# Optimization experiments

Hardware: AMD Instinct MI355X
Metric: run time of the kernel (lower is better)

The kernel has to match this reference:

```python
import jax, jax.numpy as jnp
import numpy as np

D = 192          # d_model
H = 8            # n_heads
DH = D // H      # d_head = 24
DFF = 2 * D      # FeedForward hidden = d_model*2
SIZES = [384 + 8 * i for i in range(32)]   # ragged segment lengths
TOTAL = sum(SIZES)                          # 16256
EPS = 1e-5

# static ragged -> padded index maps (numpy, baked at trace time)
_sz = np.asarray(SIZES)
B = len(_sz)
MAXN = int(_sz.max())
SEG = np.repeat(np.arange(B), _sz)                      # [TOTAL] segment id
POS = np.concatenate([np.arange(s) for s in _sz])       # [TOTAL] position in segment
PADMASK = np.ones((B, MAXN), dtype=bool)                # True = padding (key_padding_mask)
PADMASK[SEG, POS] = False


def _layernorm(x, gamma, beta):
    mu = jnp.mean(x, axis=-1, keepdims=True)
    var = jnp.var(x, axis=-1, keepdims=True)
    return (x - mu) * jax.lax.rsqrt(var + EPS) * gamma + beta


def setup_inputs() -> dict:
    key = jax.random.key(0)
    ks = jax.random.split(key, 8)
    w = lambda k, shape: jax.random.normal(k, shape, jnp.float32) * 0.02
    return {
        "x": jax.random.normal(ks[0], (TOTAL, D), jnp.float32),
        "sizes": jnp.asarray(SIZES, jnp.int32),
        "Wqkv": w(ks[1], (3 * D, D)), "bqkv": jnp.zeros((3 * D,), jnp.float32),
        "Wo": w(ks[2], (D, D)),       "bo": jnp.zeros((D,), jnp.float32),
        "Wg": w(ks[3], (D, 2 * D)),   "bg": jnp.zeros((D,), jnp.float32),
        "gamma1": jnp.ones((D,), jnp.float32), "beta1": jnp.zeros((D,), jnp.float32),
        "W1": w(ks[4], (DFF, D)),     "b1": jnp.zeros((DFF,), jnp.float32),
        "W2": w(ks[5], (D, DFF)),     "b2": jnp.zeros((D,), jnp.float32),
        "gamma2": jnp.ones((D,), jnp.float32), "beta2": jnp.zeros((D,), jnp.float32),
    }


def reference(x, sizes, Wqkv, bqkv, Wo, bo, Wg, bg, gamma1, beta1,
              W1, b1, W2, b2, gamma2, beta2):
    # --- pad_by_sizes (vectorized scatter, static index maps) ---
    pad = jnp.zeros((B, MAXN, D), x.dtype).at[SEG, POS].set(x)   # [B, MAXN, D]

    # --- nn.MultiheadAttention (batch_first, key_padding_mask) ---
    qkv = pad @ Wqkv.T + bqkv                                    # [B, MAXN, 3D]
    q, k, v = jnp.split(qkv, 3, axis=-1)
    def heads(t):  # [B, MAXN, D] -> [B, H, MAXN, DH]
        return t.reshape(B, MAXN, H, DH).transpose(0, 2, 1, 3)
    q, k, v = heads(q), heads(k), heads(v)
    scores = jnp.einsum("bhqd,bhkd->bhqk", q, k) / np.sqrt(DH)   # [B, H, MAXN, MAXN]
    scores = jnp.where(PADMASK[:, None, None, :], jnp.float32(-1e9), scores)
    attn = jax.nn.softmax(scores, axis=-1)
    o = jnp.einsum("bhqk,bhkd->bhqd", attn, v)                   # [B, H, MAXN, DH]
    o = o.transpose(0, 2, 1, 3).reshape(B, MAXN, D)
    out = o @ Wo.T + bo                                          # [B, MAXN, D]

    # --- gather back to ragged; gate/norm/ff are per-token, so the torch
    # per-segment loop is equivalent to one vectorized pass over all tokens ---
    out_flat = out[SEG, POS]                                     # [TOTAL, D]
    g = jax.nn.sigmoid(jnp.concatenate([out_flat, x], axis=-1) @ Wg.T + bg)
    h = g * out_flat + (1.0 - g) * x                             # GatedResidual
    h = _layernorm(h, gamma1, beta1)                             # self.norm
    y = jax.nn.silu(h @ W1.T + b1) @ W2.T + b2                   # FeedForward.net
    return _layernorm(h + y, gamma2, beta2)                      # residual + norm
```

## Files before the change

kernel.cpp:

```cpp
#include <hip/hip_runtime.h>
#include <math.h>

#define D_      192
#define H_      8
#define DH_     24
#define NSEG    32
#define TOTAL_  16256
static constexpr float LN_EPS = 1e-5f;
static constexpr float SCALE  = 0.20412414523193154f;
static constexpr float SC_L2E = 0.29446679331797463f;

typedef float  f32x4  __attribute__((ext_vector_type(4)));
typedef short  bf16x8 __attribute__((ext_vector_type(8)));
typedef unsigned short u16x4 __attribute__((ext_vector_type(4)));

__device__ __forceinline__ unsigned short f2b(float f) {
    union { float f; unsigned u; } v; v.f = f;
    unsigned r = v.u + 0x7FFFu + ((v.u >> 16) & 1u);
    return (unsigned short)(r >> 16);
}
__device__ __forceinline__ unsigned short f2b_fast(float f) {
    union { float f; unsigned u; } v; v.f = f;
    return (unsigned short)((v.u + 0x8000u) >> 16);
}
__device__ __forceinline__ float b2f(unsigned short h) {
    union { unsigned u; float f; } v; v.u = (unsigned)h << 16; return v.f;
}
__device__ __forceinline__ float fexp2(float x) {
#if __has_builtin(__builtin_amdgcn_exp2f)
    return __builtin_amdgcn_exp2f(x);
#else
    return exp2f(x);
#endif
}
__device__ __forceinline__ bf16x8 ldpack8(const float* p) {
    float4 a0 = *(const float4*)p;
    float4 a1 = *(const float4*)(p + 4);
    bf16x8 r;
    ((unsigned short*)&r)[0] = f2b(a0.x); ((unsigned short*)&r)[1] = f2b(a0.y);
    ((unsigned short*)&r)[2] = f2b(a0.z); ((unsigned short*)&r)[3] = f2b(a0.w);
    ((unsigned short*)&r)[4] = f2b(a1.x); ((unsigned short*)&r)[5] = f2b(a1.y);
    ((unsigned short*)&r)[6] = f2b(a1.z); ((unsigned short*)&r)[7] = f2b(a1.w);
    return r;
}

__global__ __launch_bounds__(256)
void conv_w(const float* __restrict__ w0, const float* __restrict__ w1,
            const float* __restrict__ w2, const float* __restrict__ w3,
            const float* __restrict__ w4, unsigned short* __restrict__ out)
{
    int i = (blockIdx.x * 256 + threadIdx.x) * 4;
    const float* src; int off;
    if      (i < 110592) { src = w0; off = 0; }
    else if (i < 147456) { src = w1; off = 110592; }
    else if (i < 221184) { src = w2; off = 147456; }
    else if (i < 294912) { src = w3; off = 221184; }
    else                 { src = w4; off = 294912; }
    float4 v = *(const float4*)&src[i - off];
    u16x4 o = { f2b(v.x), f2b(v.y), f2b(v.z), f2b(v.w) };
    *(u16x4*)&out[i] = o;
}

template<int KF, int MR, int OUT_BF16, int AF32>
__global__ __launch_bounds__(256)
void gemm_lds(const void* __restrict__ Ain,
              const unsigned short* __restrict__ Wb,
              const float* __restrict__ bias,
              void* __restrict__ Cout, int N)
{
    constexpr int KSW = KF * 32 + 8;
    __shared__ unsigned short Wp[64 * KSW];

    const int tid = threadIdx.x;
    const int wv  = tid >> 6;
    const int l   = tid & 63;
    const int m0  = blockIdx.x * (64 * MR) + wv * (16 * MR);
    const int n0  = blockIdx.y * 64;
    const int rl  = l & 15;
    const int kc  = (l >> 4) * 8;

    bf16x8 afrag[MR][KF];
    #pragma unroll
    for (int h = 0; h < MR; ++h)
        #pragma unroll
        for (int kk = 0; kk < KF; ++kk) {
            if (AF32)
                afrag[h][kk] = ldpack8((const float*)Ain + (size_t)(m0 + h * 16 + rl) * (KF * 32) + kk * 32 + kc);
            else
                afrag[h][kk] = *(const bf16x8*)((const unsigned short*)Ain + (size_t)(m0 + h * 16 + rl) * (KF * 32) + kk * 32 + kc);
        }

    #pragma unroll
    for (int i = 0; i < KF; ++i) {
        int u = i * 256 + tid;
        int row = u / (KF * 4), c = u % (KF * 4);
        *(bf16x8*)&Wp[row * KSW + c * 8] = *(const bf16x8*)&Wb[(size_t)(n0 + row) * (KF * 32) + c * 8];
    }
    __syncthreads();

    f32x4 acc[MR][4] = {};
    #pragma unroll
    for (int kk = 0; kk < KF; ++kk) {
        #pragma unroll
        for (int nf = 0; nf < 4; ++nf) {
            bf16x8 b = *(const bf16x8*)&Wp[(nf * 16 + rl) * KSW + kk * 32 + kc];
            #pragma unroll
            for (int h = 0; h < MR; ++h)
                acc[h][nf] = __builtin_amdgcn_mfma_f32_16x16x32_bf16(afrag[h][kk], b, acc[h][nf], 0, 0, 0);
        }
    }

    #pragma unroll
    for (int h = 0; h < MR; ++h) {
        #pragma unroll
        for (int nf = 0; nf < 4; ++nf) {
            const int c = n0 + nf * 16 + rl;
            const float bz = bias[c];
            #pragma unroll
            for (int q = 0; q < 4; ++q) {
                const int r = m0 + h * 16 + (l >> 4) * 4 + q;
                float v = acc[h][nf][q] + bz;
                if (OUT_BF16) ((unsigned short*)Cout)[(size_t)r * N + c] = f2b(v);
                else          ((float*)Cout)[(size_t)r * N + c] = v;
            }
        }
    }
}

__global__ __launch_bounds__(256, 1)
void wo_gate_ln1(const unsigned short* __restrict__ o_b,
                 const float* __restrict__ x,
                 const unsigned short* __restrict__ wo_b,
                 const unsigned short* __restrict__ wg_b,
                 const float* __restrict__ bo, const float* __restrict__ bg,
                 const float* __restrict__ gamma1, const float* __restrict__ beta1,
                 float* __restrict__ h1, unsigned short* __restrict__ h1b)
{
    constexpr int WS = 200;
    constexpr int AS = 200;
    __shared__ unsigned short Wp[192 * WS];
    __shared__ unsigned short Al[64 * AS];

    const int tid = threadIdx.x;
    const int wv  = tid >> 6;
    const int l   = tid & 63;
    const int rl  = l & 15;
    const int g   = l >> 4;
    const int kc  = g * 8;
    const int blk0 = blockIdx.x * 64;
    const int m0   = blk0 + wv * 16;

    bf16x8 afA[6];
    #pragma unroll
    for (int kk = 0; kk < 6; ++kk)
        afA[kk] = *(const bf16x8*)&o_b[(size_t)(m0 + rl) * 192 + kk * 32 + kc];

    #pragma unroll
    for (int i = 0; i < 18; ++i) {
        int u = i * 256 + tid;
        int row = u / 24, c = u % 24;
        *(bf16x8*)&Wp[row * WS + c * 8] = *(const bf16x8*)&wo_b[(size_t)row * 192 + c * 8];
    }
    __syncthreads();

    f32x4 accA[12] = {};
    #pragma unroll
    for (int kk = 0; kk < 6; ++kk)
        #pragma unroll
        for (int nf = 0; nf < 12; ++nf) {
            bf16x8 b = *(const bf16x8*)&Wp[(nf * 16 + rl) * WS + kk * 32 + kc];
            accA[nf] = __builtin_amdgcn_mfma_f32_16x16x32_bf16(afA[kk], b, accA[nf], 0, 0, 0);
        }

    float att[12][4];
    #pragma unroll
    for (int nf = 0; nf < 12; ++nf) {
        const float bz = bo[nf * 16 + rl];
        #pragma unroll
        for (int q = 0; q < 4; ++q) {
            att[nf][q] = accA[nf][q] + bz;
            const int row = wv * 16 + g * 4 + q;
            Al[row * AS + nf * 16 + rl] = f2b(att[nf][q]);
        }
    }
    __syncthreads();

    #pragma unroll
    for (int i = 0; i < 18; ++i) {
        int u = i * 256 + tid;
        int row = u / 24, c = u % 24;
        *(bf16x8*)&Wp[row * WS + c * 8] = *(const bf16x8*)&wg_b[(size_t)row * 384 + c * 8];
    }
    __syncthreads();

    f32x4 accB[12] = {};
    #pragma unroll
    for (int kk = 0; kk < 6; ++kk) {
        bf16x8 a = *(const bf16x8*)&Al[(wv * 16 + rl) * AS + kk * 32 + kc];
        #pragma unroll
        for (int nf = 0; nf < 12; ++nf) {
            bf16x8 b = *(const bf16x8*)&Wp[(nf * 16 + rl) * WS + kk * 32 + kc];
            accB[nf] = __builtin_amdgcn_mfma_f32_16x16x32_bf16(a, b, accB[nf], 0, 0, 0);
        }
    }
    __syncthreads();

    #pragma unroll
    for (int i = 0; i < 18; ++i) {
        int u = i * 256 + tid;
        int row = u / 24, c = u % 24;
        *(bf16x8*)&Wp[row * WS + c * 8] = *(const bf16x8*)&wg_b[(size_t)row * 384 + 192 + c * 8];
    }
    __syncthreads();

    #pragma unroll
    for (int kk = 0; kk < 6; ++kk) {
        bf16x8 a = ldpack8(&x[(size_t)(m0 + rl) * 192 + kk * 32 + kc]);
        #pragma unroll
        for (int nf = 0; nf < 12; ++nf) {
            bf16x8 b = *(const bf16x8*)&Wp[(nf * 16 + rl) * WS + kk * 32 + kc];
            accB[nf] = __builtin_amdgcn_mfma_f32_16x16x32_bf16(a, b, accB[nf], 0, 0, 0);
        }
    }

    float bz[12], gam[12], bet[12];
    #pragma unroll
    for (int nf = 0; nf < 12; ++nf) {
        bz[nf]  = bg[nf * 16 + rl];
        gam[nf] = gamma1[nf * 16 + rl];
        bet[nf] = beta1[nf * 16 + rl];
    }
    #pragma unroll
    for (int q = 0; q < 4; ++q) {
        const int r = m0 + g * 4 + q;
        const size_t rb = (size_t)r * 192;
        float h[12];
        float s = 0.f;
        #pragma unroll
        for (int nf = 0; nf < 12; ++nf) {
            const int c = nf * 16 + rl;
            float v  = accB[nf][q] + bz[nf];
            float gt = 1.f / (1.f + __expf(-v));
            h[nf] = gt * att[nf][q] + (1.f - gt) * x[rb + c];
            s += h[nf];
        }
        s += __shfl_xor(s, 1); s += __shfl_xor(s, 2);
        s += __shfl_xor(s, 4); s += __shfl_xor(s, 8);
        const float mu = s * (1.f / 192.f);
        float sq = 0.f;
        #pragma unroll
        for (int nf = 0; nf < 12; ++nf) { float d = h[nf] - mu; sq += d * d; }
        sq += __shfl_xor(sq, 1); sq += __shfl_xor(sq, 2);
        sq += __shfl_xor(sq, 4); sq += __shfl_xor(sq, 8);
        const float rstd = rsqrtf(sq * (1.f / 192.f) + LN_EPS);
        #pragma unroll
        for (int nf = 0; nf < 12; ++nf) {
            const int c = nf * 16 + rl;
            float rv = (h[nf] - mu) * rstd * gam[nf] + bet[nf];
            h1[rb + c]  = rv;
            h1b[rb + c] = f2b(rv);
        }
    }
}

__global__ __launch_bounds__(256, 1)
void ffn_ln2(const unsigned short* __restrict__ h1b,
             const float* __restrict__ h1,
             const unsigned short* __restrict__ w1_b,
             const unsigned short* __restrict__ w2_b,
             const float* __restrict__ b1, const float* __restrict__ b2,
             const float* __restrict__ gamma2, const float* __restrict__ beta2,
             float* __restrict__ out)
{
    constexpr int WS = 200;
    constexpr int FS = 392;
    __shared__ unsigned short Wp[192 * WS];
    __shared__ unsigned short Fl[64 * FS];

    const int tid = threadIdx.x;
    const int wv  = tid >> 6;
    const int l   = tid & 63;
    const int rl  = l & 15;
    const int g   = l >> 4;
    const int kc  = g * 8;
    const int blk0 = blockIdx.x * 64;
    const int m0   = blk0 + wv * 16;

    bf16x8 afC[6];
    #pragma unroll
    for (int kk = 0; kk < 6; ++kk)
        afC[kk] = *(const bf16x8*)&h1b[(size_t)(m0 + rl) * 192 + kk * 32 + kc];

    f32x4 accC[24] = {};
    #pragma unroll
    for (int ch = 0; ch < 2; ++ch) {
        if (ch) __syncthreads();
        #pragma unroll
        for (int i = 0; i < 18; ++i) {
            int u = i * 256 + tid;
            int row = u / 24, c = u % 24;
            *(bf16x8*)&Wp[row * WS + c * 8] = *(const bf16x8*)&w1_b[(size_t)(ch * 192 + row) * 192 + c * 8];
        }
        __syncthreads();
        #pragma unroll
        for (int kk = 0; kk < 6; ++kk)
            #pragma unroll
            for (int nf = 0; nf < 12; ++nf) {
                bf16x8 b = *(const bf16x8*)&Wp[(nf * 16 + rl) * WS + kk * 32 + kc];
                accC[ch * 12 + nf] = __builtin_amdgcn_mfma_f32_16x16x32_bf16(afC[kk], b, accC[ch * 12 + nf], 0, 0, 0);
            }
    }
    #pragma unroll
    for (int ch = 0; ch < 2; ++ch)
        #pragma unroll
        for (int nf = 0; nf < 12; ++nf) {
            const int col = ch * 192 + nf * 16 + rl;
            const float bz = b1[col];
            #pragma unroll
            for (int q = 0; q < 4; ++q) {
                float v = accC[ch * 12 + nf][q] + bz;
                float s = 1.f / (1.f + __expf(-v));
                const int row = wv * 16 + g * 4 + q;
                Fl[row * FS + col] = f2b(v * s);
            }
        }
    __syncthreads();

    f32x4 accD[12] = {};
    #pragma unroll
    for (int ch = 0; ch < 2; ++ch) {
        if (ch) __syncthreads();
        #pragma unroll
        for (int i = 0; i < 18; ++i) {
            int u = i * 256 + tid;
            int row = u / 24, c = u % 24;
            *(bf16x8*)&Wp[row * WS + c * 8] = *(const bf16x8*)&w2_b[(size_t)row * 384 + ch * 192 + c * 8];
        }
        __syncthreads();
        #pragma unroll
        for (int kk = 0; kk < 6; ++kk) {
            bf16x8 a = *(const bf16x8*)&Fl[(wv * 16 + rl) * FS + ch * 192 + kk * 32 + kc];
            #pragma unroll
            for (int nf = 0; nf < 12; ++nf) {
                bf16x8 b = *(const bf16x8*)&Wp[(nf * 16 + rl) * WS + kk * 32 + kc];
                accD[nf] = __builtin_amdgcn_mfma_f32_16x16x32_bf16(a, b, accD[nf], 0, 0, 0);
            }
        }
    }

    float bz[12], gam[12], bet[12];
    #pragma unroll
    for (int nf = 0; nf < 12; ++nf) {
        bz[nf]  = b2[nf * 16 + rl];
        gam[nf] = gamma2[nf * 16 + rl];
        bet[nf] = beta2[nf * 16 + rl];
    }
    #pragma unroll
    for (int q = 0; q < 4; ++q) {
        const int r = m0 + g * 4 + q;
        const size_t rb = (size_t)r * 192;
        float h[12];
        float s = 0.f;
        #pragma unroll
        for (int nf = 0; nf < 12; ++nf) {
            const int c = nf * 16 + rl;
            h[nf] = h1[rb + c] + accD[nf][q] + bz[nf];
            s += h[nf];
        }
        s += __shfl_xor(s, 1); s += __shfl_xor(s, 2);
        s += __shfl_xor(s, 4); s += __shfl_xor(s, 8);
        const float mu = s * (1.f / 192.f);
        float sq = 0.f;
        #pragma unroll
        for (int nf = 0; nf < 12; ++nf) { float d = h[nf] - mu; sq += d * d; }
        sq += __shfl_xor(sq, 1); sq += __shfl_xor(sq, 2);
        sq += __shfl_xor(sq, 4); sq += __shfl_xor(sq, 8);
        const float rstd = rsqrtf(sq * (1.f / 192.f) + LN_EPS);
        #pragma unroll
        for (int nf = 0; nf < 12; ++nf) {
            const int c = nf * 16 + rl;
            out[rb + c] = (h[nf] - mu) * rstd * gam[nf] + bet[nf];
        }
    }
}

#define KSTR 40
#define VSTR 72
#define PSTR 72

__global__ __launch_bounds__(256)
void attn_mfma(const unsigned short* __restrict__ qkv, unsigned short* __restrict__ o)
{
    const int seg  = blockIdx.z;
    const int head = blockIdx.y;
    const int n    = 384 + 8 * seg;
    const int base = 384 * seg + 4 * seg * (seg - 1);
    const int q0   = blockIdx.x * 128;
    if (q0 >= n) return;

    __shared__ unsigned short Ks[64 * KSTR];
    __shared__ unsigned short Vt[32 * VSTR];
    __shared__ unsigned short Pl[4][32 * PSTR];

    const int tid = threadIdx.x;
    const int wv  = tid >> 6;
    const int l   = tid & 63;
    const int lq  = l & 15;
    const int g   = l >> 4;

    if (tid < 64) *(uint4*)&Ks[tid * KSTR + 24] = make_uint4(0, 0, 0, 0);
    for (int t4 = tid; t4 < 144; t4 += 256)
        *(unsigned long long*)&Vt[24 * VSTR + t4 * 4] = 0ull;

    int   qrow[2];
    bf16x8 qfrag[2];
    #pragma unroll
    for (int qf = 0; qf < 2; ++qf) {
        qrow[qf] = q0 + wv * 32 + qf * 16 + lq;
        const int qtok = base + (qrow[qf] < n ? qrow[qf] : n - 1);
        bf16x8 qz = {};
        if (g < 3) qz = *(const bf16x8*)&qkv[(size_t)qtok * 576 + head * 24 + g * 8];
        qfrag[qf] = qz;
    }

    float lsum[2] = {0.f, 0.f};
    f32x4 oacc[2][2] = {};

    const int nt = (n + 63) >> 6;
    for (int t = 0; t < nt; ++t) {
        const int j0 = t * 64;
        __syncthreads();
        if (tid < 192) {
            const int j = tid & 63;
            const int c = tid >> 6;
            int jr = j0 + j; if (jr >= n) jr = n - 1;
            const unsigned short* rp = &qkv[(size_t)(base + jr) * 576 + head * 24 + c * 8];
            bf16x8 kv = *(const bf16x8*)(rp + 192);
            *(bf16x8*)&Ks[j * KSTR + c * 8] = kv;
            bf16x8 vv = *(const bf16x8*)(rp + 384);
            #pragma unroll
            for (int e = 0; e < 8; ++e)
                Vt[(c * 8 + e) * VSTR + j] = ((const unsigned short*)&vv)[e];
        }
        __syncthreads();

        const int rem = n - j0;
        #pragma unroll
        for (int qf = 0; qf < 2; ++qf) {
            f32x4 sacc[4] = {};
            #pragma unroll
            for (int ks = 0; ks < 4; ++ks) {
                bf16x8 kf = *(const bf16x8*)&Ks[(ks * 16 + lq) * KSTR + g * 8];
                sacc[ks] = __builtin_amdgcn_mfma_f32_16x16x32_bf16(kf, qfrag[qf], sacc[ks], 0, 0, 0);
            }
            float psum = 0.f;
            unsigned short pb[16];
            #pragma unroll
            for (int ks = 0; ks < 4; ++ks) {
                #pragma unroll
                for (int r = 0; r < 4; ++r) {
                    float p = fexp2(sacc[ks][r] * SC_L2E);
                    if (rem < 64) { int key = ks * 16 + g * 4 + r; if (key >= rem) p = 0.f; }
                    psum += p;
                    pb[ks * 4 + r] = f2b_fast(p);
                }
            }
            psum += __shfl_xor(psum, 16);
            psum += __shfl_xor(psum, 32);
            lsum[qf] += psum;
            #pragma unroll
            for (int ks = 0; ks < 4; ++ks) {
                u16x4 w4 = { pb[ks*4+0], pb[ks*4+1], pb[ks*4+2], pb[ks*4+3] };
                *(u16x4*)&Pl[wv][(qf * 16 + lq) * PSTR + ks * 16 + g * 4] = w4;
            }
        }
        asm volatile("s_waitcnt lgkmcnt(0)" ::: "memory");
        __builtin_amdgcn_sched_barrier(0);

        #pragma unroll
        for (int jk = 0; jk < 2; ++jk) {
            bf16x8 vf[2];
            #pragma unroll
            for (int df = 0; df < 2; ++df)
                vf[df] = *(const bf16x8*)&Vt[(df * 16 + lq) * VSTR + jk * 32 + g * 8];
            #pragma unroll
            for (int qf = 0; qf < 2; ++qf) {
                bf16x8 pf = *(const bf16x8*)&Pl[wv][(qf * 16 + lq) * PSTR + jk * 32 + g * 8];
                #pragma unroll
                for (int df = 0; df < 2; ++df)
                    oacc[qf][df] = __builtin_amdgcn_mfma_f32_16x16x32_bf16(vf[df], pf, oacc[qf][df], 0, 0, 0);
            }
        }
    }

    #pragma unroll
    for (int qf = 0; qf < 2; ++qf) {
        if (qrow[qf] < n) {
            const float rl2 = 1.f / lsum[qf];
            #pragma unroll
            for (int df = 0; df < 2; ++df) {
                const int d0 = df * 16 + g * 4;
                if (d0 < 24) {
                    u16x4 r = { f2b_fast(oacc[qf][df][0] * rl2), f2b_fast(oacc[qf][df][1] * rl2),
                                f2b_fast(oacc[qf][df][2] * rl2), f2b_fast(oacc[qf][df][3] * rl2) };
                    *(u16x4*)&o[(size_t)(base + qrow[qf]) * 192 + head * 24 + d0] = r;
                }
            }
        }
    }
}

extern "C" void kernel_launch(void* const* d_in, const int* in_sizes, int n_in,
                              void* d_out, int out_size, void* d_ws, size_t ws_size,
                              hipStream_t stream)
{
    const float* x      = (const float*)d_in[0];
    const float* Wqkv   = (const float*)d_in[2];
    const float* bqkv   = (const float*)d_in[3];
    const float* Wo     = (const float*)d_in[4];
    const float* bo     = (const float*)d_in[5];
    const float* Wg     = (const float*)d_in[6];
    const float* bg     = (const float*)d_in[7];
    const float* gamma1 = (const float*)d_in[8];
    const float* beta1  = (const float*)d_in[9];
    const float* W1     = (const float*)d_in[10];
    const float* b1     = (const float*)d_in[11];
    const float* W2     = (const float*)d_in[12];
    const float* b2     = (const float*)d_in[13];
    const float* gamma2 = (const float*)d_in[14];
    const float* beta2  = (const float*)d_in[15];
    float* out = (float*)d_out;
    float* ws  = (float*)d_ws;

    const size_t T = TOTAL_;
    unsigned short* qkv_b = (unsigned short*)ws;
    unsigned short* o_b   = (unsigned short*)(ws + 288 * T);
    float*          h1    = ws + 384 * T;
    unsigned short* h1b   = (unsigned short*)(ws + 576 * T);
    unsigned short* wb    = (unsigned short*)(ws + 672 * T);

    dim3 blk(256);

    conv_w<<<dim3(360), blk, 0, stream>>>(Wqkv, Wo, Wg, W1, W2, wb);
    gemm_lds<6,2,1,1><<<dim3(127, 9), blk, 0, stream>>>(x, wb, bqkv, qkv_b, 576);
    attn_mfma<<<dim3(5, H_, NSEG), blk, 0, stream>>>(qkv_b, o_b);
    wo_gate_ln1<<<dim3(254), blk, 0, stream>>>(o_b, x, wb + 110592, wb + 147456,
                                               bo, bg, gamma1, beta1, h1, h1b);
    ffn_ln2<<<dim3(254), blk, 0, stream>>>(h1b, h1, wb + 221184, wb + 294912,
                                           b1, b2, gamma2, beta2, out);
}
```

Measured before the change: 105.1 us.

## Keep attention P in registers via permuted V layout; pre-convert x to bf16

In the attention kernel, the softmax probabilities are packed straight into registers as the B operand of the PV MFMA. This removes the per-wave LDS round trip and its waitcnt barrier, and works because V is stored transposed with a column permutation that matches the accumulator layout of the score MFMA. K fragments are also hoisted out of the q-fragment loop. Separately, x is converted to bf16 once in the weight-conversion kernel, so the QKV GEMM loads bf16 directly instead of converting fp32 in every one of its 9 column blocks. That adds an extra pass over x and a larger conversion launch.

```diff
diff --git a/kernel.cpp b/kernel.cpp
--- a/kernel.cpp
+++ b/kernel.cpp
@@ -13,11 +13,16 @@
 typedef float  f32x4  __attribute__((ext_vector_type(4)));
 typedef short  bf16x8 __attribute__((ext_vector_type(8)));
 typedef unsigned short u16x4 __attribute__((ext_vector_type(4)));
+typedef unsigned int   u32x4 __attribute__((ext_vector_type(4)));
 
 __device__ __forceinline__ unsigned short f2b(float f) {
     union { float f; unsigned u; } v; v.f = f;
     unsigned r = v.u + 0x7FFFu + ((v.u >> 16) & 1u);
     return (unsigned short)(r >> 16);
+}
+__device__ __forceinline__ unsigned f2b_u32(float f) {
+    union { float f; unsigned u; } v; v.f = f;
+    return (v.u + 0x8000u) >> 16;
 }
 __device__ __forceinline__ unsigned short f2b_fast(float f) {
     union { float f; unsigned u; } v; v.f = f;
@@ -44,26 +49,34 @@
     return r;
 }
 
+#define NXE 3121152
 __global__ __launch_bounds__(256)
-void conv_w(const float* __restrict__ w0, const float* __restrict__ w1,
-            const float* __restrict__ w2, const float* __restrict__ w3,
-            const float* __restrict__ w4, unsigned short* __restrict__ out)
+void conv_all(const float* __restrict__ x,
+              const float* __restrict__ w0, const float* __restrict__ w1,
+              const float* __restrict__ w2, const float* __restrict__ w3,
+              const float* __restrict__ w4,
+              unsigned short* __restrict__ xb, unsigned short* __restrict__ wb)
 {
     int i = (blockIdx.x * 256 + threadIdx.x) * 4;
-    const float* src; int off;
-    if      (i < 110592) { src = w0; off = 0; }
-    else if (i < 147456) { src = w1; off = 110592; }
-    else if (i < 221184) { src = w2; off = 147456; }
-    else if (i < 294912) { src = w3; off = 221184; }
-    else                 { src = w4; off = 294912; }
+    const float* src; unsigned short* dst; int off;
+    if (i < NXE) { src = x; dst = xb; off = 0; }
+    else {
+        int j = i - NXE; dst = wb;
+        if      (j < 110592) { src = w0; off = 0; }
+        else if (j < 147456) { src = w1; off = 110592; }
+        else if (j < 221184) { src = w2; off = 147456; }
+        else if (j < 294912) { src = w3; off = 221184; }
+        else                 { src = w4; off = 294912; }
+        i = j;
+    }
     float4 v = *(const float4*)&src[i - off];
     u16x4 o = { f2b(v.x), f2b(v.y), f2b(v.z), f2b(v.w) };
-    *(u16x4*)&out[i] = o;
-}
-
-template<int KF, int MR, int OUT_BF16, int AF32>
+    *(u16x4*)&dst[i] = o;
+}
+
+template<int KF, int MR, int OUT_BF16>
 __global__ __launch_bounds__(256)
-void gemm_lds(const void* __restrict__ Ain,
+void gemm_lds(const unsigned short* __restrict__ Ain,
               const unsigned short* __restrict__ Wb,
               const float* __restrict__ bias,
               void* __restrict__ Cout, int N)
@@ -83,12 +96,8 @@
     #pragma unroll
     for (int h = 0; h < MR; ++h)
         #pragma unroll
-        for (int kk = 0; kk < KF; ++kk) {
-            if (AF32)
-                afrag[h][kk] = ldpack8((const float*)Ain + (size_t)(m0 + h * 16 + rl) * (KF * 32) + kk * 32 + kc);
-            else
-                afrag[h][kk] = *(const bf16x8*)((const unsigned short*)Ain + (size_t)(m0 + h * 16 + rl) * (KF * 32) + kk * 32 + kc);
-        }
+        for (int kk = 0; kk < KF; ++kk)
+            afrag[h][kk] = *(const bf16x8*)&Ain[(size_t)(m0 + h * 16 + rl) * (KF * 32) + kk * 32 + kc];
 
     #pragma unroll
     for (int i = 0; i < KF; ++i) {
@@ -147,8 +156,7 @@
     const int rl  = l & 15;
     const int g   = l >> 4;
     const int kc  = g * 8;
-    const int blk0 = blockIdx.x * 64;
-    const int m0   = blk0 + wv * 16;
+    const int m0  = blockIdx.x * 64 + wv * 16;
 
     bf16x8 afA[6];
     #pragma unroll
@@ -283,8 +291,7 @@
     const int rl  = l & 15;
     const int g   = l >> 4;
     const int kc  = g * 8;
-    const int blk0 = blockIdx.x * 64;
-    const int m0   = blk0 + wv * 16;
+    const int m0  = blockIdx.x * 64 + wv * 16;
 
     bf16x8 afC[6];
     #pragma unroll
@@ -386,7 +393,6 @@
 
 #define KSTR 40
 #define VSTR 72
-#define PSTR 72
 
 __global__ __launch_bounds__(256)
 void attn_mfma(const unsigned short* __restrict__ qkv, unsigned short* __restrict__ o)
@@ -400,7 +406,6 @@
 
     __shared__ unsigned short Ks[64 * KSTR];
     __shared__ unsigned short Vt[32 * VSTR];
-    __shared__ unsigned short Pl[4][32 * PSTR];
 
     const int tid = threadIdx.x;
     const int wv  = tid >> 6;
@@ -433,6 +438,7 @@
         if (tid < 192) {
             const int j = tid & 63;
             const int c = tid >> 6;
+            const int cj = 32 * (j >> 5) + 8 * ((j >> 2) & 3) + 4 * ((j >> 4) & 1) + (j & 3);
             int jr = j0 + j; if (jr >= n) jr = n - 1;
             const unsigned short* rp = &qkv[(size_t)(base + jr) * 576 + head * 24 + c * 8];
             bf16x8 kv = *(const bf16x8*)(rp + 192);
@@ -440,42 +446,48 @@
             bf16x8 vv = *(const bf16x8*)(rp + 384);
             #pragma unroll
             for (int e = 0; e < 8; ++e)
-                Vt[(c * 8 + e) * VSTR + j] = ((const unsigned short*)&vv)[e];
+                Vt[(c * 8 + e) * VSTR + cj] = ((const unsigned short*)&vv)[e];
         }
         __syncthreads();
 
+        bf16x8 kf[4];
+        #pragma unroll
+        for (int ks = 0; ks < 4; ++ks)
+            kf[ks] = *(const bf16x8*)&Ks[(ks * 16 + lq) * KSTR + g * 8];
+
         const int rem = n - j0;
+        bf16x8 pfr[2][2];
         #pragma unroll
         for (int qf = 0; qf < 2; ++qf) {
             f32x4 sacc[4] = {};
             #pragma unroll
+            for (int ks = 0; ks < 4; ++ks)
+                sacc[ks] = __builtin_amdgcn_mfma_f32_16x16x32_bf16(kf[ks], qfrag[qf], sacc[ks], 0, 0, 0);
+
+            float psum = 0.f;
+            unsigned pw[8];
+            #pragma unroll
             for (int ks = 0; ks < 4; ++ks) {
-                bf16x8 kf = *(const bf16x8*)&Ks[(ks * 16 + lq) * KSTR + g * 8];
-                sacc[ks] = __builtin_amdgcn_mfma_f32_16x16x32_bf16(kf, qfrag[qf], sacc[ks], 0, 0, 0);
-            }
-            float psum = 0.f;
-            unsigned short pb[16];
-            #pragma unroll
-            for (int ks = 0; ks < 4; ++ks) {
+                float pv[4];
                 #pragma unroll
                 for (int r = 0; r < 4; ++r) {
                     float p = fexp2(sacc[ks][r] * SC_L2E);
                     if (rem < 64) { int key = ks * 16 + g * 4 + r; if (key >= rem) p = 0.f; }
                     psum += p;
-                    pb[ks * 4 + r] = f2b_fast(p);
+                    pv[r] = p;
                 }
+                pw[ks * 2 + 0] = f2b_u32(pv[0]) | (f2b_u32(pv[1]) << 16);
+                pw[ks * 2 + 1] = f2b_u32(pv[2]) | (f2b_u32(pv[3]) << 16);
             }
             psum += __shfl_xor(psum, 16);
             psum += __shfl_xor(psum, 32);
             lsum[qf] += psum;
             #pragma unroll
-            for (int ks = 0; ks < 4; ++ks) {
-                u16x4 w4 = { pb[ks*4+0], pb[ks*4+1], pb[ks*4+2], pb[ks*4+3] };
-                *(u16x4*)&Pl[wv][(qf * 16 + lq) * PSTR + ks * 16 + g * 4] = w4;
-            }
-        }
-        asm volatile("s_waitcnt lgkmcnt(0)" ::: "memory");
-        __builtin_amdgcn_sched_barrier(0);
+            for (int jk = 0; jk < 2; ++jk) {
+                u32x4 fr = { pw[jk*4+0], pw[jk*4+1], pw[jk*4+2], pw[jk*4+3] };
+                pfr[qf][jk] = *(bf16x8*)&fr;
+            }
+        }
 
         #pragma unroll
         for (int jk = 0; jk < 2; ++jk) {
@@ -484,12 +496,10 @@
             for (int df = 0; df < 2; ++df)
                 vf[df] = *(const bf16x8*)&Vt[(df * 16 + lq) * VSTR + jk * 32 + g * 8];
             #pragma unroll
-            for (int qf = 0; qf < 2; ++qf) {
-                bf16x8 pf = *(const bf16x8*)&Pl[wv][(qf * 16 + lq) * PSTR + jk * 32 + g * 8];
+            for (int qf = 0; qf < 2; ++qf)
                 #pragma unroll
                 for (int df = 0; df < 2; ++df)
-                    oacc[qf][df] = __builtin_amdgcn_mfma_f32_16x16x32_bf16(vf[df], pf, oacc[qf][df], 0, 0, 0);
-            }
+                    oacc[qf][df] = __builtin_amdgcn_mfma_f32_16x16x32_bf16(vf[df], pfr[qf][jk], oacc[qf][df], 0, 0, 0);
         }
     }
 
@@ -538,11 +548,12 @@
     float*          h1    = ws + 384 * T;
     unsigned short* h1b   = (unsigned short*)(ws + 576 * T);
     unsigned short* wb    = (unsigned short*)(ws + 672 * T);
+    unsigned short* xb    = (unsigned short*)(ws + 684 * T);
 
     dim3 blk(256);
 
-    conv_w<<<dim3(360), blk, 0, stream>>>(Wqkv, Wo, Wg, W1, W2, wb);
-    gemm_lds<6,2,1,1><<<dim3(127, 9), blk, 0, stream>>>(x, wb, bqkv, qkv_b, 576);
+    conv_all<<<dim3(3408), blk, 0, stream>>>(x, Wqkv, Wo, Wg, W1, W2, xb, wb);
+    gemm_lds<6,2,1><<<dim3(127, 9), blk, 0, stream>>>(xb, wb, bqkv, qkv_b, 576);
     attn_mfma<<<dim3(5, H_, NSEG), blk, 0, stream>>>(qkv_b, o_b);
     wo_gate_ln1<<<dim3(254), blk, 0, stream>>>(o_b, x, wb + 110592, wb + 147456,
                                                bo, bg, gamma1, beta1, h1, h1b);
```

Result: faster. 97.69 us (-7.1%).
